# Kernel optimization log

Measured on AMD Instinct MI355X. Metric: run time of the kernel, lower is better.

## Reference

```python
import jax, jax.numpy as jnp
import numpy as np

N, E, G = 16384, 65536, 512
T, FIN, FOUT = 4, 128, 32
_DEG_HIST = np.array([1.0, 2.0, 3.0, 4.0])
AVG_LOG = float((np.log(np.arange(4) + 1.0) * _DEG_HIST).sum() / _DEG_HIST.sum())


def _bn(x, g, b, eps=1e-5):
    # BatchNorm1d in training mode: biased batch stats
    m = x.mean(0)
    v = x.var(0)
    return (x - m) * jax.lax.rsqrt(v + eps) * g + b


def _pna_conv(x, edge_index, ea_raw, We_c, be_c, Wpre, bpre, Wpost, bpost, Wlin, blin):
    src, dst = edge_index[0], edge_index[1]
    ea = ea_raw @ We_c + be_c                                   # conv-internal edge encoder [E,FIN]
    xt = jnp.broadcast_to(x[:, None, :], (N, T, FIN))           # towers share input (divide_input=False)
    h = jnp.concatenate([xt[dst], xt[src],
                         jnp.broadcast_to(ea[:, None, :], (E, T, FIN))], axis=-1)  # [E,T,3*FIN]
    m = jnp.einsum('etf,tfg->etg', h, Wpre) + bpre              # per-tower pre-NN [E,T,FIN]
    deg = jnp.clip(jax.ops.segment_sum(jnp.ones((E,), x.dtype), dst, N), 1.0)
    inv = (1.0 / deg)[:, None, None]
    mean = jax.ops.segment_sum(m, dst, N) * inv
    mean2 = jax.ops.segment_sum(m * m, dst, N) * inv
    std = jnp.sqrt(jax.nn.relu(mean2 - mean * mean) + 1e-5)
    mn = jax.ops.segment_min(m, dst, N)
    mx = jax.ops.segment_max(m, dst, N)
    mn = jnp.where(jnp.isfinite(mn), mn, 0.0)
    mx = jnp.where(jnp.isfinite(mx), mx, 0.0)
    agg = jnp.concatenate([mean, mn, mx, std], axis=-1)         # [N,T,4*FIN]
    s = (jnp.log(deg + 1.0) / AVG_LOG)[:, None, None]           # amplification scaler
    out = jnp.concatenate([agg, agg * s, agg / s], axis=-1)     # identity|amp|attenuation [N,T,12*FIN]
    out = jnp.concatenate([xt, out], axis=-1)                   # [N,T,13*FIN]
    out = jnp.einsum('ntf,tfg->ntg', out, Wpost) + bpost        # per-tower post-NN [N,T,FOUT]
    return out.reshape(N, T * FOUT) @ Wlin + blin               # tower mixing [N,FIN]


def setup_inputs() -> dict:
    key = jax.random.key(0)
    ks = jax.random.split(key, 24)
    def rn(k, shape, scale=0.05):
        return jax.random.normal(k, shape, dtype=jnp.float32) * scale
    return dict(
        x=jax.random.normal(ks[0], (N, 11), jnp.float32),
        edge_attr=jax.random.uniform(ks[1], (E, 4), jnp.float32),
        edge_index=jax.random.randint(ks[2], (2, E), 0, N),
        batch=jnp.sort(jax.random.randint(ks[3], (N,), 0, G)),
        Wa=rn(ks[4], (11, FIN), 0.2), ba=rn(ks[5], (FIN,)),
        We=rn(ks[6], (4, FIN), 0.2), be=rn(ks[7], (FIN,)),
        We_conv=rn(ks[8], (3, FIN, FIN)), be_conv=rn(ks[9], (3, FIN)),
        Wpre=rn(ks[10], (3, T, 3 * FIN, FIN)), bpre=rn(ks[11], (3, T, FIN)),
        Wpost=rn(ks[12], (3, T, 13 * FIN, FOUT)), bpost=rn(ks[13], (3, T, FOUT)),
        Wlin=rn(ks[14], (3, FIN, FIN)), blin=rn(ks[15], (3, FIN)),
        bng=1.0 + rn(ks[16], (3, FIN)), bnb=rn(ks[17], (3, FIN)),
        W1=rn(ks[18], (FIN, 64), 0.1), b1=rn(ks[19], (64,)),
        hg=1.0 + rn(ks[20], (64,)), hb=rn(ks[21], (64,)),
        W2=rn(ks[22], (64, 1), 0.1), b2=rn(ks[23], (1,)),
    )


def reference(x, edge_attr, edge_index, batch, Wa, ba, We, be,
              We_conv, be_conv, Wpre, bpre, Wpost, bpost, Wlin, blin,
              bng, bnb, W1, b1, hg, hb, W2, b2):
    h = jax.nn.relu(x @ Wa + ba)
    ea = jax.nn.relu(edge_attr @ We + be)
    for l in range(3):
        h = jax.nn.relu(_bn(_pna_conv(h, edge_index, ea, We_conv[l], be_conv[l],
                                      Wpre[l], bpre[l], Wpost[l], bpost[l],
                                      Wlin[l], blin[l]), bng[l], bnb[l]))
    cnt = jnp.clip(jax.ops.segment_sum(jnp.ones((N,), h.dtype), batch, G), 1.0)
    pooled = jax.ops.segment_sum(h, batch, G) / cnt[:, None]    # global_mean_pool
    z = jax.nn.relu(pooled @ W1 + b1)
    z = _bn(z, hg, hb)
    return (z @ W2 + b2).reshape(-1)
```

## Files before the change

kernel.cpp:

```cpp
#include <hip/hip_runtime.h>
#include <hip/hip_bf16.h>

#define DEVFN static __device__ __forceinline__

constexpr int NN = 16384;
constexpr int EE = 65536;
constexpr int GG = 512;
constexpr float AVG_LOG_F = 1.0227308671603782f;

typedef _Float16 hfrag __attribute__((ext_vector_type(8)));
typedef __attribute__((ext_vector_type(4))) float f4;
typedef __attribute__((ext_vector_type(8))) unsigned short us8v;

DEVFN unsigned short f2h(float f) {
  _Float16 h = (_Float16)f;
  unsigned short r; __builtin_memcpy(&r, &h, 2); return r;
}
DEVFN float h2f(unsigned short s) {
  _Float16 h; __builtin_memcpy(&h, &s, 2); return (float)h;
}

DEVFN float4 ld4hf(const unsigned short* p) {
  ushort4 u = *(const ushort4*)p;
  float4 r;
  r.x = h2f(u.x); r.y = h2f(u.y); r.z = h2f(u.z); r.w = h2f(u.w);
  return r;
}
DEVFN void ld8hf(const unsigned short* p, float* o) {
  us8v v = *(const us8v*)p;
#pragma unroll
  for (int i = 0; i < 8; ++i) o[i] = h2f(v[i]);
}

DEVFN int swk(int row, int k) {
  return (k & ~31) + ((((k >> 3) & 3) ^ ((row >> 1) & 3)) << 3) + (k & 7);
}

DEVFN void gll16(const unsigned short* g, unsigned short* l) {
  __builtin_amdgcn_global_load_lds(
      (__attribute__((address_space(1))) void*)g,
      (__attribute__((address_space(3))) void*)l, 16, 0, 0);
}

struct AuxP {
  const float* p0;
  const float* p1;
  const float* p2;
  const float* p3;
  const float* p4;
};

__global__ __launch_bounds__(256) void abc_gemm(
    const unsigned short* __restrict__ hbf, const unsigned short* __restrict__ preABT_l,
    unsigned short* __restrict__ AB,
    const unsigned short* __restrict__ eaf, const unsigned short* __restrict__ foldT_l,
    const float* __restrict__ bfold_l, unsigned short* __restrict__ Mb)
{
  __shared__ __align__(16) unsigned short S[16384];
  unsigned short* AhS = S;
  unsigned short* BhS = S + 8192;

  const int bid = blockIdx.x;
  const unsigned short* Abase;
  const unsigned short* Wbase;
  const float* bias = nullptr;
  unsigned short* Cu;
  int ldc, bn;
  long long bm;
  if (bid < 1024) {
    const int z = bid >> 8, y = (bid >> 7) & 1, xm = bid & 127;
    Abase = hbf;
    Wbase = preABT_l + (size_t)z * 256 * 128;
    Cu = AB + (size_t)z * NN * 256;
    ldc = 256; bn = y * 128; bm = (long long)xm * 128;
  } else {
    const int idx = bid - 1024;
    const int z = idx >> 9, xm = idx & 511;
    Abase = eaf;
    Wbase = foldT_l + (size_t)z * 128 * 128;
    bias = bfold_l + z * 128;
    Cu = Mb + (size_t)z * EE * 128;
    ldc = 128; bn = 0; bm = (long long)xm * 128;
  }

  const int tid = threadIdx.x;
  const int w = tid >> 6;
  const int lane = tid & 63;
  const int quad = lane >> 4;
  const int c16 = lane & 15;
  const int srow = lane >> 2;
  const int sslot = (lane & 3) << 3;

  f4 acc[2][8];
#pragma unroll
  for (int mt = 0; mt < 2; ++mt)
#pragma unroll
    for (int nt = 0; nt < 8; ++nt) acc[mt][nt] = (f4){0.f, 0.f, 0.f, 0.f};

  const unsigned short* whp = Wbase + (long long)(bn + srow) * 128 + sslot;
  const unsigned short* ahp = Abase + (bm + srow) * 128 + sslot;
  const int swr8 = ((quad ^ ((c16 >> 1) & 3)) << 3);

  auto stage = [&](int bi, int k0) {
#pragma unroll
    for (int ch = w; ch < 8; ch += 4) {
      gll16(ahp + (long long)ch * 16 * 128 + k0, AhS + bi * 4096 + ch * 512);
      gll16(whp + (long long)ch * 16 * 128 + k0, BhS + bi * 4096 + ch * 512);
    }
  };
  auto fragmfma = [&](int bi) {
    hfrag ah[2];
#pragma unroll
    for (int mt = 0; mt < 2; ++mt)
      ah[mt] = *(const hfrag*)&AhS[bi * 4096 + (w * 32 + mt * 16 + c16) * 32 + swr8];
#pragma unroll
    for (int nt = 0; nt < 8; ++nt) {
      hfrag bh = *(const hfrag*)&BhS[bi * 4096 + (nt * 16 + c16) * 32 + swr8];
#pragma unroll
      for (int mt = 0; mt < 2; ++mt)
        acc[mt][nt] = __builtin_amdgcn_mfma_f32_16x16x32_f16(ah[mt], bh, acc[mt][nt], 0, 0, 0);
    }
  };

  stage(0, 0);
  __syncthreads();
#pragma unroll
  for (int kt = 0; kt < 4; ++kt) {
    const int bi = kt & 1;
    if (kt < 3) stage(bi ^ 1, (kt + 1) << 5);
    fragmfma(bi);
    __syncthreads();
  }

#pragma unroll
  for (int nt = 0; nt < 8; ++nt) {
    const int colL = nt * 16 + c16;
    const float bv = bias ? bias[colL] : 0.f;
#pragma unroll
    for (int mt = 0; mt < 2; ++mt) {
#pragma unroll
      for (int r = 0; r < 4; ++r) {
        const int row = w * 32 + mt * 16 + quad * 4 + r;
        S[row * 128 + colL] = f2h(acc[mt][nt][r] + bv);
      }
    }
  }
  __syncthreads();
#pragma unroll
  for (int p = 0; p < 8; ++p) {
    const int row = p * 16 + (tid >> 4);
    const int co = (tid & 15) * 8;
    *(uint4*)&Cu[(bm + row) * ldc + bn + co] = *(const uint4*)&S[row * 128 + co];
  }
}

template <int ASRC, int NT, bool BIAS, bool RELU, bool OHALF>
__global__ __launch_bounds__(256) void mgemm(
    const void* __restrict__ Av, const unsigned short* __restrict__ WT,
    const float* __restrict__ bias,
    float* __restrict__ C, AuxP aux,
    int Nc, int K, int lda, int ldc,
    long long bsA, long long bsW, long long bsC, int bsBias)
{
  constexpr bool COPYA = (ASRC == 1);
  constexpr int BST = NT * 16 * 32;

  const int z = blockIdx.z;
  WT += (long long)z * bsW;
  if (BIAS) bias += (long long)z * bsBias;
  float* Cf = C + (OHALF ? 0 : (long long)z * bsC);
  unsigned short* Cu = (unsigned short*)C + (OHALF ? (long long)z * bsC : 0);

  __shared__ __align__(16) unsigned short AhS[2 * 128 * 32];
  __shared__ __align__(16) unsigned short BhS[2 * BST];

  const int tid = threadIdx.x;
  const long long bm = (long long)blockIdx.x * 128;
  const int bn = blockIdx.y * (NT * 16);
  const int w = tid >> 6;
  const int lane = tid & 63;
  const int quad = lane >> 4;
  const int c16 = lane & 15;
  const int srow = lane >> 2;
  const int sslot = (lane & 3) << 3;

  const int arow = tid >> 1;
  const int sel = tid & 1;
  const long long rowsrc = bm + arow;

  f4 acc[2][NT];
#pragma unroll
  for (int mt = 0; mt < 2; ++mt)
#pragma unroll
    for (int nt = 0; nt < NT; ++nt) acc[mt][nt] = (f4){0.f, 0.f, 0.f, 0.f};

  const unsigned short* whp = WT + (long long)(bn + srow) * K + sslot;

  const unsigned short* ahp = nullptr;
  if (COPYA || ASRC == 3)
    ahp = (const unsigned short*)Av + (long long)z * bsA + (bm + srow) * (long long)lda + sslot;

  float invdc = 1.f;
  float sv = 0.f, iv = 0.f;
  const float* apA = nullptr;
  const unsigned short* Prow_base = nullptr;
  if (ASRC == 3) {
    Prow_base = (const unsigned short*)aux.p0 + rowsrc * 384;
    sv = aux.p2[rowsrc];
    iv = aux.p3[rowsrc];
  } else if (ASRC == 4) {
    apA = (const float*)Av + (long long)z * bsA + rowsrc * lda;
    invdc = 1.f / fmaxf(aux.p0[rowsrc], 1.f);
  }
  const int swa = (arow >> 1) & 3;
  const int s0us = arow * 32 + (((2 * sel) ^ swa) << 3);
  const int s1us = arow * 32 + (((2 * sel + 1) ^ swa) << 3);

  const int swr8 = ((quad ^ ((c16 >> 1) & 3)) << 3);

  auto stageB = [&](int bi, int k0) {
#pragma unroll
    for (int ch = w; ch < NT; ch += 4)
      gll16(whp + (long long)ch * 16 * K + k0, BhS + bi * BST + ch * 512);
  };
  auto stageA = [&](int bi, int k0) {
#pragma unroll
    for (int ch = w; ch < 8; ch += 4)
      gll16(ahp + (long long)ch * 16 * lda + k0, AhS + bi * 4096 + ch * 512);
  };
  auto stageLoad = [&](int k0, float* va) {
    const int ck0 = k0 + sel * 16;
    if (ASRC == 3) {
      const unsigned short* Prow = Prow_base + ((ck0 >> 5) * 96) + (ck0 & 31);
      float pid[16], pam[16], pat[16];
      ld8hf(Prow, pid); ld8hf(Prow + 8, pid + 8);
      ld8hf(Prow + 32, pam); ld8hf(Prow + 40, pam + 8);
      ld8hf(Prow + 64, pat); ld8hf(Prow + 72, pat + 8);
#pragma unroll
      for (int i = 0; i < 16; ++i)
        va[i] = pid[i] + sv * pam[i] + iv * pat[i] + aux.p4[ck0 + i];
    } else {
      *(float4*)&va[0] = *(const float4*)(apA + ck0);
      *(float4*)&va[4] = *(const float4*)(apA + ck0 + 4);
      *(float4*)&va[8] = *(const float4*)(apA + ck0 + 8);
      *(float4*)&va[12] = *(const float4*)(apA + ck0 + 12);
    }
  };
  auto stageWrite = [&](int bi, const float* va) {
    hfrag hv0, hv1;
#pragma unroll
    for (int i = 0; i < 16; ++i) {
      float x = va[i];
      if (ASRC == 4) x *= invdc;
      if (i < 8) hv0[i] = (_Float16)x;
      else       hv1[i - 8] = (_Float16)x;
    }
    *(hfrag*)&AhS[bi * 4096 + s0us] = hv0;
    *(hfrag*)&AhS[bi * 4096 + s1us] = hv1;
  };
  auto fragmfma = [&](int bi) {
    hfrag ah[2];
#pragma unroll
    for (int mt = 0; mt < 2; ++mt) {
      const int r = w * 32 + mt * 16 + c16;
      ah[mt] = *(const hfrag*)&AhS[bi * 4096 + r * 32 + swr8];
    }
#pragma unroll
    for (int nt = 0; nt < NT; ++nt) {
      const int r = nt * 16 + c16;
      hfrag bh = *(const hfrag*)&BhS[bi * BST + r * 32 + swr8];
#pragma unroll
      for (int mt = 0; mt < 2; ++mt)
        acc[mt][nt] = __builtin_amdgcn_mfma_f32_16x16x32_f16(ah[mt], bh, acc[mt][nt], 0, 0, 0);
    }
  };

  float va[16];
  const int nk = K >> 5;

  if (COPYA) {
    stageA(0, 0);
    stageB(0, 0);
  } else {
    stageLoad(0, va);
    stageB(0, 0);
    stageWrite(0, va);
  }
  __syncthreads();

  for (int kt = 0; kt < nk; ++kt) {
    const int bi = kt & 1;
    const bool pf = (kt + 1 < nk);
    bool nextds = false;
    if (pf) {
      const int k0 = (kt + 1) << 5;
      stageB(bi ^ 1, k0);
      if (COPYA) {
        stageA(bi ^ 1, k0);
      } else if (ASRC == 3 && k0 >= 128) {
        stageA(bi ^ 1, k0 - 128);
      } else {
        stageLoad(k0, va);
        nextds = true;
      }
    }
    fragmfma(bi);
    if (nextds) stageWrite(bi ^ 1, va);
    __syncthreads();
  }

  float ls[NT], lq[NT];
#pragma unroll
  for (int nt = 0; nt < NT; ++nt) { ls[nt] = 0.f; lq[nt] = 0.f; }
#pragma unroll
  for (int nt = 0; nt < NT; ++nt) {
    int col = bn + nt * 16 + c16;
    if (col >= Nc) continue;
    float bv = BIAS ? bias[col] : 0.f;
#pragma unroll
    for (int mt = 0; mt < 2; ++mt) {
#pragma unroll
      for (int r = 0; r < 4; ++r) {
        long long row = bm + w * 32 + mt * 16 + quad * 4 + r;
        float v = acc[mt][nt][r] + bv;
        if (RELU) v = fmaxf(v, 0.f);
        if (ASRC == 3) { ls[nt] += v; lq[nt] += v * v; }
        if (OHALF) Cu[row * ldc + col] = f2h(v);
        else Cf[row * ldc + col] = v;
      }
    }
  }
  if constexpr (ASRC == 3) {
    float* csum = (float*)AhS;
    float* csq = csum + 128;
    if (tid < 128) { csum[tid] = 0.f; csq[tid] = 0.f; }
    __syncthreads();
#pragma unroll
    for (int nt = 0; nt < NT; ++nt) {
      int col = bn + nt * 16 + c16;
      atomicAdd(&csum[col], ls[nt]);
      atomicAdd(&csq[col], lq[nt]);
    }
    __syncthreads();
    float* colsum = (float*)aux.p1;
    if (tid < 128) {
      atomicAdd(&colsum[tid], csum[tid]);
      atomicAdd(&colsum[128 + tid], csq[tid]);
    }
  }
}

__global__ __launch_bounds__(256) void edge_enc(
    const float* __restrict__ eat, const float* __restrict__ We,
    const float* __restrict__ be, const int* __restrict__ slot_of,
    unsigned short* __restrict__ ef)
{
  int e = blockIdx.x * 2 + (threadIdx.x >> 7);
  int c = threadIdx.x & 127;
  float acc = be[c];
#pragma unroll
  for (int k = 0; k < 4; ++k) acc += eat[e * 4 + k] * We[k * 128 + c];
  long long slot = slot_of[e];
  ef[slot * 128 + swk((int)slot, c)] = f2h(fmaxf(acc, 0.f));
}

__global__ void count_deg(const int* __restrict__ dst, int* __restrict__ degi)
{
  int e = blockIdx.x * 256 + threadIdx.x;
  if (e < EE) atomicAdd(&degi[dst[e]], 1);
}

__global__ __launch_bounds__(1024) void scan_k(const int* __restrict__ degi,
                                               int* __restrict__ row_off,
                                               int* __restrict__ cursor,
                                               float* __restrict__ s_arr,
                                               float* __restrict__ invs)
{
  __shared__ int tsum[1024];
  int t = threadIdx.x;
  int local[16];
  int base = t * 16;
  int s = 0;
#pragma unroll
  for (int i = 0; i < 16; ++i) { local[i] = s; s += degi[base + i]; }
  tsum[t] = s;
  __syncthreads();
  for (int off = 1; off < 1024; off <<= 1) {
    int v = (t >= off) ? tsum[t - off] : 0;
    __syncthreads();
    tsum[t] += v;
    __syncthreads();
  }
  int prev = (t == 0) ? 0 : tsum[t - 1];
#pragma unroll
  for (int i = 0; i < 16; ++i) {
    int start = prev + local[i];
    row_off[base + i] = start;
    cursor[base + i] = start;
    int cnt = degi[base + i];
    float degc = fmaxf((float)cnt, 1.f);
    float sv = logf(degc + 1.f) / AVG_LOG_F;
    s_arr[base + i] = sv;
    invs[base + i] = 1.f / sv;
  }
  if (t == 1023) row_off[NN] = tsum[1023];
}

__global__ void scatter_k(const int* __restrict__ src, const int* __restrict__ dst,
                          int* __restrict__ cursor,
                          int* __restrict__ slot_of, int* __restrict__ esrc)
{
  int e = blockIdx.x * 256 + threadIdx.x;
  if (e >= EE) return;
  int d = dst[e];
  int slot = atomicAdd(&cursor[d], 1);
  slot_of[e] = slot;
  esrc[slot] = src[e];
}

__global__ __launch_bounds__(512) void fold_w(const float* __restrict__ We_conv,
                                              const float* __restrict__ Wpre,
                                              float* __restrict__ Wfold)
{
  int k = blockIdx.x & 127, l = blockIdx.x >> 7;
  int t = threadIdx.x >> 7, f = threadIdx.x & 127;
  const float* wc = We_conv + (long long)(l * 128 + k) * 128;
  const float* wp = Wpre + ((long long)((l * 4 + t) * 384 + 256)) * 128 + f;
  float acc = 0.f;
  for (int j = 0; j < 128; ++j) acc += wc[j] * wp[(long long)j * 128];
  Wfold[((long long)(l * 128 + k)) * 512 + threadIdx.x] = acc;
}

__global__ __launch_bounds__(512) void fold_b(const float* __restrict__ be_conv,
                                              const float* __restrict__ Wpre,
                                              const float* __restrict__ bpre,
                                              float* __restrict__ bfold)
{
  int l = blockIdx.x;
  int t = threadIdx.x >> 7, f = threadIdx.x & 127;
  const float* bc = be_conv + l * 128;
  const float* wp = Wpre + ((long long)((l * 4 + t) * 384 + 256)) * 128 + f;
  float acc = bpre[(l * 4 + t) * 128 + f];
  for (int j = 0; j < 128; ++j) acc += bc[j] * wp[(long long)j * 128];
  bfold[l * 512 + threadIdx.x] = acc;
}

__global__ __launch_bounds__(128) void pack_all(
    const float* __restrict__ Wpre, const float* __restrict__ WfoldF,
    const float* __restrict__ Wpost, const float* __restrict__ Wlin,
    const float* __restrict__ W1,
    const float* __restrict__ x, const float* __restrict__ Wa,
    const float* __restrict__ ba,
    unsigned short* __restrict__ preABT, unsigned short* __restrict__ foldT,
    unsigned short* __restrict__ post3T, unsigned short* __restrict__ linT2,
    unsigned short* __restrict__ w1T, unsigned short* __restrict__ hbf)
{
  const int b = blockIdx.x;
  const int t = threadIdx.x;
  if (b < 3072) {
    int lt = b >> 8, n = b & 255, k = t;
    int row = (n < 128) ? k : (128 + k);
    int f = n & 127;
    float v = Wpre[((long long)(lt * 384 + row)) * 128 + f];
    preABT[((long long)(lt * 256 + n)) * 128 + swk(n, k)] = f2h(v);
  } else if (b < 4608) {
    int b2 = b - 3072;
    int lt = b2 >> 7, n = b2 & 127, k = t;
    int l = lt >> 2, tw = lt & 3;
    float v = WfoldF[((long long)(l * 128 + k)) * 512 + tw * 128 + n];
    foldT[((long long)(lt * 128 + n)) * 128 + swk(n, k)] = f2h(v);
  } else if (b < 6144) {
    int b3 = b - 4608;
    int lt = b3 >> 7, c = b3 & 127;
#pragma unroll
    for (int j = 0; j < 4; ++j) {
      int r = t + 128 * j;
      float v = 0.f;
      if (c < 96)
        v = Wpost[((long long)(lt * 1664 + 128 + (c >> 5) * 512 + r)) * 32 + (c & 31)];
      post3T[((long long)(lt * 128 + c)) * 512 + swk(c, r)] = f2h(v);
    }
  } else if (b < 6528) {
    int b4 = b - 6144;
    int l = b4 >> 7, n = b4 & 127, k = t;
    float v = Wlin[((long long)(l * 128 + k)) * 128 + n];
    linT2[((long long)(l * 128 + n)) * 256 + swk(n, k)] = f2h(v);
  } else if (b < 6912) {
    int b5 = b - 6528;
    int l = b5 >> 7, kk = b5 & 127, o = t;
    float acc = 0.f;
    for (int c = 0; c < 128; ++c) {
      float wx = Wpost[((long long)((l * 4 + (c >> 5)) * 1664 + kk)) * 32 + (c & 31)];
      acc += wx * Wlin[((long long)(l * 128 + c)) * 128 + o];
    }
    linT2[((long long)(l * 128 + o)) * 256 + swk(o, 128 + kk)] = f2h(acc);
  } else if (b < 6976) {
    int n = b - 6912, k = t;
    w1T[(long long)n * 128 + swk(n, k)] = f2h(W1[k * 64 + n]);
  } else {
    int n = b - 6976, c = t;
    float acc = ba[c];
#pragma unroll
    for (int k = 0; k < 11; ++k) acc += x[n * 11 + k] * Wa[k * 128 + c];
    hbf[((long long)n << 7) + swk(n, c)] = f2h(fmaxf(acc, 0.f));
  }
}

__global__ __launch_bounds__(256) void aggregate_ct(
    const unsigned short* __restrict__ ABb, const unsigned short* __restrict__ Mb,
    const int* __restrict__ row_off, const int* __restrict__ esrc,
    unsigned short* __restrict__ aggs)
{
  const int tid = threadIdx.x;
  const int c8 = (tid & 15) << 3;
  const int z = (tid >> 4) & 3;
  const int n = blockIdx.x * 4 + (tid >> 6);
  const unsigned short* M = Mb + (long long)z * EE * 128;
  const unsigned short* ABs = ABb + (long long)z * NN * 256;
  unsigned short* ag = aggs + (long long)z * NN * 512;
  const int beg = row_off[n], end = row_off[n + 1];
  const int cnt = end - beg;
  const float degc = fmaxf((float)cnt, 1.0f);
  float aval[8];
  ld8hf(&ABs[(long long)n * 256 + c8], aval);

  float sum[8], sq[8], mn[8], mx[8];
#pragma unroll
  for (int j = 0; j < 8; ++j) {
    sum[j] = 0.f; sq[j] = 0.f; mn[j] = INFINITY; mx[j] = -INFINITY;
  }

  auto upd = [&](const float* mv, const float* bv) {
#pragma unroll
    for (int j = 0; j < 8; ++j) {
      float m = aval[j] + bv[j] + mv[j];
      sum[j] += m; sq[j] += m * m;
      mn[j] = fminf(mn[j], m); mx[j] = fmaxf(mx[j], m);
    }
  };

  for (int s0 = beg; s0 < end; s0 += 4) {
    const int e1 = min(s0 + 1, end - 1);
    const int e2 = min(s0 + 2, end - 1);
    const int e3 = min(s0 + 3, end - 1);
    const int sA = esrc[s0], sB = esrc[e1], sC = esrc[e2], sD = esrc[e3];
    float mA[8], mB[8], mC[8], mD[8], bA[8], bB[8], bC[8], bD[8];
    ld8hf(&M[(long long)s0 * 128 + c8], mA);
    ld8hf(&M[(long long)e1 * 128 + c8], mB);
    ld8hf(&M[(long long)e2 * 128 + c8], mC);
    ld8hf(&M[(long long)e3 * 128 + c8], mD);
    ld8hf(&ABs[(long long)sA * 256 + 128 + c8], bA);
    ld8hf(&ABs[(long long)sB * 256 + 128 + c8], bB);
    ld8hf(&ABs[(long long)sC * 256 + 128 + c8], bC);
    ld8hf(&ABs[(long long)sD * 256 + 128 + c8], bD);
    upd(mA, bA);
    if (s0 + 1 < end) upd(mB, bB);
    if (s0 + 2 < end) upd(mC, bC);
    if (s0 + 3 < end) upd(mD, bD);
  }

  const float inv = 1.0f / degc;
  us8v omean, omin, omax, ostd;
#pragma unroll
  for (int j = 0; j < 8; ++j) {
    float mean = sum[j] * inv;
    float var = sq[j] * inv - mean * mean;
    float stdv = sqrtf(fmaxf(var, 0.f) + 1e-5f);
    float mnv = (cnt > 0) ? mn[j] : 0.f;
    float mxv = (cnt > 0) ? mx[j] : 0.f;
    omean[j] = f2h(mean);
    omin[j] = f2h(mnv);
    omax[j] = f2h(mxv);
    ostd[j] = f2h(stdv);
  }
  const int sc = swk(n, c8);
  const long long base = (long long)n * 512 + sc;
  *(us8v*)&ag[base] = omean;
  *(us8v*)&ag[base + 128] = omin;
  *(us8v*)&ag[base + 256] = omax;
  *(us8v*)&ag[base + 384] = ostd;
}

__global__ __launch_bounds__(256) void bn_apply(const unsigned short* __restrict__ hn,
                                                const float* __restrict__ cs,
                                                const float* __restrict__ g,
                                                const float* __restrict__ b,
                                                unsigned short* __restrict__ hb)
{
  int idx = blockIdx.x * 256 + threadIdx.x;
  int c = idx & 127, n = idx >> 7;
  float mean = cs[c] * (1.f / 16384.f);
  float var = cs[128 + c] * (1.f / 16384.f) - mean * mean;
  float sc = g[c] * rsqrtf(var + 1e-5f);
  float v = fmaxf(h2f(hn[idx]) * sc + (b[c] - mean * sc), 0.f);
  hb[((long long)n << 7) + swk(n, c)] = f2h(v);
}

__global__ void pool_add(const unsigned short* __restrict__ y, const float* __restrict__ cs,
                         const float* __restrict__ g, const float* __restrict__ b,
                         const int* __restrict__ batch,
                         float* __restrict__ pooled, float* __restrict__ cntf)
{
  int n = blockIdx.x, c = threadIdx.x;
  float mean = cs[c] * (1.f / 16384.f);
  float var = cs[128 + c] * (1.f / 16384.f) - mean * mean;
  float v = fmaxf((h2f(y[(long long)n * 128 + c]) - mean) * rsqrtf(var + 1e-5f) * g[c] + b[c], 0.f);
  int bb = batch[n];
  atomicAdd(&pooled[(long long)bb * 128 + c], v);
  if (c == 0) atomicAdd(&cntf[bb], 1.f);
}

__global__ __launch_bounds__(256) void zstats(const float* __restrict__ z,
                                              float* __restrict__ zm, float* __restrict__ zv)
{
  int j = blockIdx.x;
  float s = 0.f, q = 0.f;
  for (int g = threadIdx.x; g < GG; g += 256) {
    float v = z[g * 64 + j];
    s += v;
    q += v * v;
  }
  __shared__ float ps[256], pq[256];
  ps[threadIdx.x] = s;
  pq[threadIdx.x] = q;
  __syncthreads();
  for (int st = 128; st > 0; st >>= 1) {
    if (threadIdx.x < st) {
      ps[threadIdx.x] += ps[threadIdx.x + st];
      pq[threadIdx.x] += pq[threadIdx.x + st];
    }
    __syncthreads();
  }
  if (threadIdx.x == 0) {
    float m = ps[0] / (float)GG;
    zm[j] = m;
    zv[j] = pq[0] / (float)GG - m * m;
  }
}

__global__ void final_out(const float* __restrict__ z, const float* __restrict__ zm,
                          const float* __restrict__ zv, const float* __restrict__ hg,
                          const float* __restrict__ hb, const float* __restrict__ W2,
                          const float* __restrict__ b2, float* __restrict__ out)
{
  int g = blockIdx.x;
  int j = threadIdx.x;
  float v = (z[g * 64 + j] - zm[j]) * rsqrtf(zv[j] + 1e-5f) * hg[j] + hb[j];
  float t = v * W2[j];
#pragma unroll
  for (int off = 32; off > 0; off >>= 1) t += __shfl_down(t, off);
  if (j == 0) out[g] = t + b2[0];
}

extern "C" void kernel_launch(void* const* d_in, const int* in_sizes, int n_in,
                              void* d_out, int out_size, void* d_ws, size_t ws_size,
                              hipStream_t stream)
{
  (void)in_sizes; (void)n_in; (void)out_size;
  const float* x = (const float*)d_in[0];
  const float* eat = (const float*)d_in[1];
  const int* ei = (const int*)d_in[2];
  const int* batch = (const int*)d_in[3];
  const float* Wa = (const float*)d_in[4];
  const float* ba = (const float*)d_in[5];
  const float* We = (const float*)d_in[6];
  const float* be = (const float*)d_in[7];
  const float* We_conv = (const float*)d_in[8];
  const float* be_conv = (const float*)d_in[9];
  const float* Wpre = (const float*)d_in[10];
  const float* bpre = (const float*)d_in[11];
  const float* Wpost = (const float*)d_in[12];
  const float* bpost = (const float*)d_in[13];
  const float* Wlin = (const float*)d_in[14];
  const float* blin = (const float*)d_in[15];
  const float* bng = (const float*)d_in[16];
  const float* bnb = (const float*)d_in[17];
  const float* W1 = (const float*)d_in[18];
  const float* b1 = (const float*)d_in[19];
  const float* hg = (const float*)d_in[20];
  const float* hb = (const float*)d_in[21];
  const float* W2 = (const float*)d_in[22];
  const float* b2 = (const float*)d_in[23];
  float* out = (float*)d_out;

  const int* srcI = ei;
  const int* dstI = ei + EE;

  char* ws = (char*)d_ws;
  size_t off = 0;
  auto alloc = [&](size_t bytes) -> char* {
    char* p = ws + off;
    off += (bytes + 255) & ~(size_t)255;
    return p;
  };

  unsigned short* hbf = (unsigned short*)alloc((size_t)NN * 128 * 2);
  unsigned short* hn = (unsigned short*)alloc((size_t)NN * 128 * 2);
  unsigned short* eaf = (unsigned short*)alloc((size_t)EE * 128 * 2);
  unsigned short* AB = (unsigned short*)alloc((size_t)4 * NN * 256 * 2);
  char* Mregion = alloc((size_t)4 * EE * 128 * 2);
  unsigned short* Mb = (unsigned short*)Mregion;
  unsigned short* P = (unsigned short*)Mregion;
  unsigned short* aggt = (unsigned short*)alloc((size_t)4 * NN * 512 * 2);
  float* s_arr = (float*)alloc((size_t)NN * 4);
  float* invs = (float*)alloc((size_t)NN * 4);
  int* degi = (int*)alloc((size_t)NN * 4);
  int* cursor = (int*)alloc((size_t)NN * 4);
  int* row_off = (int*)alloc((size_t)(NN + 1) * 4);
  int* slot_of = (int*)alloc((size_t)EE * 4);
  int* esrc = (int*)alloc((size_t)EE * 4);
  float* WfoldF = (float*)alloc((size_t)3 * 128 * 512 * 4);
  float* bfold = (float*)alloc((size_t)3 * 512 * 4);
  unsigned short* preABT = (unsigned short*)alloc((size_t)12 * 256 * 128 * 2);
  unsigned short* foldT = (unsigned short*)alloc((size_t)12 * 128 * 128 * 2);
  unsigned short* post3T = (unsigned short*)alloc((size_t)12 * 128 * 512 * 2);
  unsigned short* linT2 = (unsigned short*)alloc((size_t)3 * 128 * 256 * 2);
  unsigned short* w1T = (unsigned short*)alloc((size_t)64 * 128 * 2);
  float* colstats = (float*)alloc(3 * 256 * 4);
  float* pooled = (float*)alloc((size_t)GG * 128 * 4);
  float* cntf = (float*)alloc((size_t)GG * 4);
  float* zbuf = (float*)alloc((size_t)GG * 64 * 4);
  float* zm = (float*)alloc(64 * 4);
  float* zv = (float*)alloc(64 * 4);

  if (off > ws_size) return;

  hipMemsetAsync(degi, 0, (size_t)NN * 4, stream);
  hipMemsetAsync(colstats, 0, 3 * 256 * 4, stream);
  count_deg<<<EE / 256, 256, 0, stream>>>(dstI, degi);
  scan_k<<<1, 1024, 0, stream>>>(degi, row_off, cursor, s_arr, invs);
  scatter_k<<<EE / 256, 256, 0, stream>>>(srcI, dstI, cursor, slot_of, esrc);

  edge_enc<<<EE / 2, 256, 0, stream>>>(eat, We, be, slot_of, eaf);
  fold_w<<<384, 512, 0, stream>>>(We_conv, Wpre, WfoldF);
  fold_b<<<3, 512, 0, stream>>>(be_conv, Wpre, bpre, bfold);
  pack_all<<<6976 + NN, 128, 0, stream>>>(Wpre, WfoldF, Wpost, Wlin, W1, x, Wa, ba,
                                          preABT, foldT, post3T, linT2, w1T, hbf);

  for (int l = 0; l < 3; ++l) {
    float* cs_l = colstats + l * 256;
    abc_gemm<<<3072, 256, 0, stream>>>(
        hbf, preABT + (size_t)l * 4 * 256 * 128, AB,
        eaf, foldT + (size_t)l * 4 * 128 * 128, bfold + l * 512, Mb);
    aggregate_ct<<<dim3(NN / 4, 1, 1), 256, 0, stream>>>(AB, Mb, row_off, esrc, aggt);
    mgemm<1, 6, false, false, true><<<dim3(NN / 128, 1, 4), 256, 0, stream>>>(
        aggt, post3T + (size_t)l * 4 * 128 * 512, nullptr, (float*)P, AuxP{},
        96, 512, 512, 384, (long long)NN * 512, (long long)128 * 512, 96, 0);
    mgemm<3, 8, true, false, true><<<dim3(NN / 128, 1, 1), 256, 0, stream>>>(
        hbf, linT2 + (size_t)l * 128 * 256, blin + l * 128, (float*)hn,
        AuxP{(const float*)P, cs_l, s_arr, invs, bpost + l * 128},
        128, 256, 128, 128, 0, 0, 0, 0);
    if (l < 2)
      bn_apply<<<NN * 128 / 256, 256, 0, stream>>>(hn, cs_l, bng + l * 128,
                                                   bnb + l * 128, hbf);
  }

  hipMemsetAsync(pooled, 0, (size_t)GG * 128 * 4, stream);
  hipMemsetAsync(cntf, 0, (size_t)GG * 4, stream);
  pool_add<<<NN, 128, 0, stream>>>(hn, colstats + 2 * 256,
                                   bng + 2 * 128, bnb + 2 * 128, batch, pooled, cntf);
  mgemm<4, 4, true, true, false><<<dim3(GG / 128, 1, 1), 256, 0, stream>>>(
      pooled, w1T, b1, zbuf, AuxP{cntf, nullptr, nullptr, nullptr, nullptr},
      64, 128, 128, 64, 0, 0, 0, 0);
  zstats<<<64, 256, 0, stream>>>(zbuf, zm, zv);
  final_out<<<GG, 64, 0, stream>>>(zbuf, zm, zv, hg, hb, W2, b2, out);
}
```

Baseline: 554.1 us.

## Fuse edge-feature GEMM into neighbor aggregation to avoid materializing per-edge messages

Splits the combined GEMM kernel so it only computes the node-side A/B projections, and moves the edge-attribute projection into the aggregation kernel. Each aggregation block computes, per 64-edge chunk of its CSR range, the edge projection with MFMA into LDS and then reduces mean/min/max/std from LDS instead of reading a precomputed per-edge buffer from global memory. This removes writing and rereading a large fp16 edge-message tensor per layer, at the cost of smaller, less efficient GEMM tiles, repeated weight staging per chunk, and extra synchronisation inside the aggregation loop.

```diff
diff --git a/kernel.cpp b/kernel.cpp
--- a/kernel.cpp
+++ b/kernel.cpp
@@ -20,12 +20,6 @@
   _Float16 h; __builtin_memcpy(&h, &s, 2); return (float)h;
 }
 
-DEVFN float4 ld4hf(const unsigned short* p) {
-  ushort4 u = *(const ushort4*)p;
-  float4 r;
-  r.x = h2f(u.x); r.y = h2f(u.y); r.z = h2f(u.z); r.w = h2f(u.w);
-  return r;
-}
 DEVFN void ld8hf(const unsigned short* p, float* o) {
   us8v v = *(const us8v*)p;
 #pragma unroll
@@ -50,38 +44,20 @@
   const float* p4;
 };
 
-__global__ __launch_bounds__(256) void abc_gemm(
+__global__ __launch_bounds__(256) void ab_gemm(
     const unsigned short* __restrict__ hbf, const unsigned short* __restrict__ preABT_l,
-    unsigned short* __restrict__ AB,
-    const unsigned short* __restrict__ eaf, const unsigned short* __restrict__ foldT_l,
-    const float* __restrict__ bfold_l, unsigned short* __restrict__ Mb)
+    unsigned short* __restrict__ AB)
 {
   __shared__ __align__(16) unsigned short S[16384];
   unsigned short* AhS = S;
   unsigned short* BhS = S + 8192;
 
   const int bid = blockIdx.x;
-  const unsigned short* Abase;
-  const unsigned short* Wbase;
-  const float* bias = nullptr;
-  unsigned short* Cu;
-  int ldc, bn;
-  long long bm;
-  if (bid < 1024) {
-    const int z = bid >> 8, y = (bid >> 7) & 1, xm = bid & 127;
-    Abase = hbf;
-    Wbase = preABT_l + (size_t)z * 256 * 128;
-    Cu = AB + (size_t)z * NN * 256;
-    ldc = 256; bn = y * 128; bm = (long long)xm * 128;
-  } else {
-    const int idx = bid - 1024;
-    const int z = idx >> 9, xm = idx & 511;
-    Abase = eaf;
-    Wbase = foldT_l + (size_t)z * 128 * 128;
-    bias = bfold_l + z * 128;
-    Cu = Mb + (size_t)z * EE * 128;
-    ldc = 128; bn = 0; bm = (long long)xm * 128;
-  }
+  const int z = bid >> 8, y = (bid >> 7) & 1, xm = bid & 127;
+  const unsigned short* Wbase = preABT_l + (size_t)z * 256 * 128;
+  unsigned short* Cu = AB + (size_t)z * NN * 256;
+  const int bn = y * 128;
+  const long long bm = (long long)xm * 128;
 
   const int tid = threadIdx.x;
   const int w = tid >> 6;
@@ -98,7 +74,7 @@
     for (int nt = 0; nt < 8; ++nt) acc[mt][nt] = (f4){0.f, 0.f, 0.f, 0.f};
 
   const unsigned short* whp = Wbase + (long long)(bn + srow) * 128 + sslot;
-  const unsigned short* ahp = Abase + (bm + srow) * 128 + sslot;
+  const unsigned short* ahp = hbf + (bm + srow) * 128 + sslot;
   const int swr8 = ((quad ^ ((c16 >> 1) & 3)) << 3);
 
   auto stage = [&](int bi, int k0) {
@@ -135,13 +111,12 @@
 #pragma unroll
   for (int nt = 0; nt < 8; ++nt) {
     const int colL = nt * 16 + c16;
-    const float bv = bias ? bias[colL] : 0.f;
 #pragma unroll
     for (int mt = 0; mt < 2; ++mt) {
 #pragma unroll
       for (int r = 0; r < 4; ++r) {
         const int row = w * 32 + mt * 16 + quad * 4 + r;
-        S[row * 128 + colL] = f2h(acc[mt][nt][r] + bv);
+        S[row * 128 + colL] = f2h(acc[mt][nt][r]);
       }
     }
   }
@@ -150,8 +125,144 @@
   for (int p = 0; p < 8; ++p) {
     const int row = p * 16 + (tid >> 4);
     const int co = (tid & 15) * 8;
-    *(uint4*)&Cu[(bm + row) * ldc + bn + co] = *(const uint4*)&S[row * 128 + co];
-  }
+    *(uint4*)&Cu[(bm + row) * 256 + bn + co] = *(const uint4*)&S[row * 128 + co];
+  }
+}
+
+__global__ __launch_bounds__(256) void aggc(
+    const unsigned short* __restrict__ eaf, const unsigned short* __restrict__ foldT_l,
+    const float* __restrict__ bfold_l, const unsigned short* __restrict__ ABb,
+    const int* __restrict__ row_off, const int* __restrict__ esrc,
+    unsigned short* __restrict__ aggs)
+{
+  __shared__ __align__(16) unsigned short AhS[2 * 2048];
+  __shared__ __align__(16) unsigned short BhS[2 * 4096];
+  __shared__ __align__(16) unsigned short Cl[64 * 128];
+
+  const int z = blockIdx.y;
+  const int n0 = blockIdx.x * 16;
+  const unsigned short* W = foldT_l + (size_t)z * 128 * 128;
+  const float* bias = bfold_l + z * 128;
+  const unsigned short* ABs = ABb + (size_t)z * NN * 256;
+  unsigned short* ag = aggs + (size_t)z * NN * 512;
+
+  const int tid = threadIdx.x;
+  const int w = tid >> 6;
+  const int lane = tid & 63;
+  const int quad = lane >> 4;
+  const int c16 = lane & 15;
+  const int srow = lane >> 2;
+  const int sslot = (lane & 3) << 3;
+  const int swr8 = ((quad ^ ((c16 >> 1) & 3)) << 3);
+
+  const int beg0 = row_off[n0];
+  const int end0 = row_off[n0 + 16];
+
+  const int wk = tid >> 4;
+  const int c8 = (tid & 15) << 3;
+  const int n = n0 + wk;
+  const int beg_n = row_off[n];
+  const int end_n = row_off[n + 1];
+  const int cnt = end_n - beg_n;
+  float aval[8];
+  ld8hf(&ABs[(long long)n * 256 + c8], aval);
+
+  float sum[8], sq[8], mn[8], mx[8];
+#pragma unroll
+  for (int j = 0; j < 8; ++j) {
+    sum[j] = 0.f; sq[j] = 0.f; mn[j] = INFINITY; mx[j] = -INFINITY;
+  }
+  auto upd = [&](const float* cv, const float* bv) {
+#pragma unroll
+    for (int j = 0; j < 8; ++j) {
+      float m = aval[j] + bv[j] + cv[j];
+      sum[j] += m; sq[j] += m * m;
+      mn[j] = fminf(mn[j], m); mx[j] = fmaxf(mx[j], m);
+    }
+  };
+
+  const unsigned short* whp = W + (long long)srow * 128 + sslot;
+
+  for (int c0 = (beg0 & ~7); c0 < end0; c0 += 64) {
+    const unsigned short* ahp = eaf + (long long)(c0 + srow) * 128 + sslot;
+    f4 acc[8];
+#pragma unroll
+    for (int nt = 0; nt < 8; ++nt) acc[nt] = (f4){0.f, 0.f, 0.f, 0.f};
+
+    auto stage = [&](int bi, int k0) {
+      gll16(ahp + (long long)(w * 16) * 128 + k0, AhS + bi * 2048 + w * 512);
+#pragma unroll
+      for (int ch = w; ch < 8; ch += 4)
+        gll16(whp + (long long)ch * 16 * 128 + k0, BhS + bi * 4096 + ch * 512);
+    };
+    stage(0, 0);
+    __syncthreads();
+#pragma unroll
+    for (int kt = 0; kt < 4; ++kt) {
+      const int bi = kt & 1;
+      if (kt < 3) stage(bi ^ 1, (kt + 1) << 5);
+      hfrag ah = *(const hfrag*)&AhS[bi * 2048 + (w * 16 + c16) * 32 + swr8];
+#pragma unroll
+      for (int nt = 0; nt < 8; ++nt) {
+        hfrag bh = *(const hfrag*)&BhS[bi * 4096 + (nt * 16 + c16) * 32 + swr8];
+        acc[nt] = __builtin_amdgcn_mfma_f32_16x16x32_f16(ah, bh, acc[nt], 0, 0, 0);
+      }
+      __syncthreads();
+    }
+#pragma unroll
+    for (int nt = 0; nt < 8; ++nt) {
+      const int col = nt * 16 + c16;
+      const float bv = bias[col];
+#pragma unroll
+      for (int r = 0; r < 4; ++r)
+        Cl[(w * 16 + quad * 4 + r) * 128 + col] = f2h(acc[nt][r] + bv);
+    }
+    __syncthreads();
+
+    const int ce = c0 + 64;
+    const int sb = max(beg_n, c0);
+    const int se = min(end_n, ce);
+    for (int s0 = sb; s0 < se; s0 += 4) {
+      const int e1 = min(s0 + 1, se - 1);
+      const int e2 = min(s0 + 2, se - 1);
+      const int e3 = min(s0 + 3, se - 1);
+      const int sA = esrc[s0], sB = esrc[e1], sC = esrc[e2], sD = esrc[e3];
+      float cA[8], cB[8], cC[8], cD[8], bA[8], bB[8], bC[8], bD[8];
+      ld8hf(&Cl[(s0 - c0) * 128 + c8], cA);
+      ld8hf(&Cl[(e1 - c0) * 128 + c8], cB);
+      ld8hf(&Cl[(e2 - c0) * 128 + c8], cC);
+      ld8hf(&Cl[(e3 - c0) * 128 + c8], cD);
+      ld8hf(&ABs[(long long)sA * 256 + 128 + c8], bA);
+      ld8hf(&ABs[(long long)sB * 256 + 128 + c8], bB);
+      ld8hf(&ABs[(long long)sC * 256 + 128 + c8], bC);
+      ld8hf(&ABs[(long long)sD * 256 + 128 + c8], bD);
+      upd(cA, bA);
+      if (s0 + 1 < se) upd(cB, bB);
+      if (s0 + 2 < se) upd(cC, bC);
+      if (s0 + 3 < se) upd(cD, bD);
+    }
+    __syncthreads();
+  }
+
+  const float degc = fmaxf((float)cnt, 1.0f);
+  const float inv = 1.0f / degc;
+  us8v omean, omin, omax, ostd;
+#pragma unroll
+  for (int j = 0; j < 8; ++j) {
+    float mean = sum[j] * inv;
+    float var = sq[j] * inv - mean * mean;
+    float stdv = sqrtf(fmaxf(var, 0.f) + 1e-5f);
+    omean[j] = f2h(mean);
+    omin[j] = f2h((cnt > 0) ? mn[j] : 0.f);
+    omax[j] = f2h((cnt > 0) ? mx[j] : 0.f);
+    ostd[j] = f2h(stdv);
+  }
+  const int sc = swk(n, c8);
+  const long long base = (long long)n * 512 + sc;
+  *(us8v*)&ag[base] = omean;
+  *(us8v*)&ag[base + 128] = omin;
+  *(us8v*)&ag[base + 256] = omax;
+  *(us8v*)&ag[base + 384] = ostd;
 }
 
 template <int ASRC, int NT, bool BIAS, bool RELU, bool OHALF>
@@ -504,81 +615,6 @@
     for (int k = 0; k < 11; ++k) acc += x[n * 11 + k] * Wa[k * 128 + c];
     hbf[((long long)n << 7) + swk(n, c)] = f2h(fmaxf(acc, 0.f));
   }
-}
-
-__global__ __launch_bounds__(256) void aggregate_ct(
-    const unsigned short* __restrict__ ABb, const unsigned short* __restrict__ Mb,
-    const int* __restrict__ row_off, const int* __restrict__ esrc,
-    unsigned short* __restrict__ aggs)
-{
-  const int tid = threadIdx.x;
-  const int c8 = (tid & 15) << 3;
-  const int z = (tid >> 4) & 3;
-  const int n = blockIdx.x * 4 + (tid >> 6);
-  const unsigned short* M = Mb + (long long)z * EE * 128;
-  const unsigned short* ABs = ABb + (long long)z * NN * 256;
-  unsigned short* ag = aggs + (long long)z * NN * 512;
-  const int beg = row_off[n], end = row_off[n + 1];
-  const int cnt = end - beg;
-  const float degc = fmaxf((float)cnt, 1.0f);
-  float aval[8];
-  ld8hf(&ABs[(long long)n * 256 + c8], aval);
-
-  float sum[8], sq[8], mn[8], mx[8];
-#pragma unroll
-  for (int j = 0; j < 8; ++j) {
-    sum[j] = 0.f; sq[j] = 0.f; mn[j] = INFINITY; mx[j] = -INFINITY;
-  }
-
-  auto upd = [&](const float* mv, const float* bv) {
-#pragma unroll
-    for (int j = 0; j < 8; ++j) {
-      float m = aval[j] + bv[j] + mv[j];
-      sum[j] += m; sq[j] += m * m;
-      mn[j] = fminf(mn[j], m); mx[j] = fmaxf(mx[j], m);
-    }
-  };
-
-  for (int s0 = beg; s0 < end; s0 += 4) {
-    const int e1 = min(s0 + 1, end - 1);
-    const int e2 = min(s0 + 2, end - 1);
-    const int e3 = min(s0 + 3, end - 1);
-    const int sA = esrc[s0], sB = esrc[e1], sC = esrc[e2], sD = esrc[e3];
-    float mA[8], mB[8], mC[8], mD[8], bA[8], bB[8], bC[8], bD[8];
-    ld8hf(&M[(long long)s0 * 128 + c8], mA);
-    ld8hf(&M[(long long)e1 * 128 + c8], mB);
-    ld8hf(&M[(long long)e2 * 128 + c8], mC);
-    ld8hf(&M[(long long)e3 * 128 + c8], mD);
-    ld8hf(&ABs[(long long)sA * 256 + 128 + c8], bA);
-    ld8hf(&ABs[(long long)sB * 256 + 128 + c8], bB);
-    ld8hf(&ABs[(long long)sC * 256 + 128 + c8], bC);
-    ld8hf(&ABs[(long long)sD * 256 + 128 + c8], bD);
-    upd(mA, bA);
-    if (s0 + 1 < end) upd(mB, bB);
-    if (s0 + 2 < end) upd(mC, bC);
-    if (s0 + 3 < end) upd(mD, bD);
-  }
-
-  const float inv = 1.0f / degc;
-  us8v omean, omin, omax, ostd;
-#pragma unroll
-  for (int j = 0; j < 8; ++j) {
-    float mean = sum[j] * inv;
-    float var = sq[j] * inv - mean * mean;
-    float stdv = sqrtf(fmaxf(var, 0.f) + 1e-5f);
-    float mnv = (cnt > 0) ? mn[j] : 0.f;
-    float mxv = (cnt > 0) ? mx[j] : 0.f;
-    omean[j] = f2h(mean);
-    omin[j] = f2h(mnv);
-    omax[j] = f2h(mxv);
-    ostd[j] = f2h(stdv);
-  }
-  const int sc = swk(n, c8);
-  const long long base = (long long)n * 512 + sc;
-  *(us8v*)&ag[base] = omean;
-  *(us8v*)&ag[base + 128] = omin;
-  *(us8v*)&ag[base + 256] = omax;
-  *(us8v*)&ag[base + 384] = ostd;
 }
 
 __global__ __launch_bounds__(256) void bn_apply(const unsigned short* __restrict__ hn,
@@ -696,11 +732,9 @@
 
   unsigned short* hbf = (unsigned short*)alloc((size_t)NN * 128 * 2);
   unsigned short* hn = (unsigned short*)alloc((size_t)NN * 128 * 2);
-  unsigned short* eaf = (unsigned short*)alloc((size_t)EE * 128 * 2);
+  unsigned short* eaf = (unsigned short*)alloc((size_t)(EE + 128) * 128 * 2);
   unsigned short* AB = (unsigned short*)alloc((size_t)4 * NN * 256 * 2);
-  char* Mregion = alloc((size_t)4 * EE * 128 * 2);
-  unsigned short* Mb = (unsigned short*)Mregion;
-  unsigned short* P = (unsigned short*)Mregion;
+  unsigned short* P = (unsigned short*)alloc((size_t)NN * 384 * 2);
   unsigned short* aggt = (unsigned short*)alloc((size_t)4 * NN * 512 * 2);
   float* s_arr = (float*)alloc((size_t)NN * 4);
   float* invs = (float*)alloc((size_t)NN * 4);
@@ -739,10 +773,10 @@
 
   for (int l = 0; l < 3; ++l) {
     float* cs_l = colstats + l * 256;
-    abc_gemm<<<3072, 256, 0, stream>>>(
-        hbf, preABT + (size_t)l * 4 * 256 * 128, AB,
-        eaf, foldT + (size_t)l * 4 * 128 * 128, bfold + l * 512, Mb);
-    aggregate_ct<<<dim3(NN / 4, 1, 1), 256, 0, stream>>>(AB, Mb, row_off, esrc, aggt);
+    ab_gemm<<<1024, 256, 0, stream>>>(hbf, preABT + (size_t)l * 4 * 256 * 128, AB);
+    aggc<<<dim3(NN / 16, 4), 256, 0, stream>>>(
+        eaf, foldT + (size_t)l * 4 * 128 * 128, bfold + l * 512,
+        AB, row_off, esrc, aggt);
     mgemm<1, 6, false, false, true><<<dim3(NN / 128, 1, 4), 256, 0, stream>>>(
         aggt, post3T + (size_t)l * 4 * 128 * 512, nullptr, (float*)P, AuxP{},
         96, 512, 512, 384, (long long)NN * 512, (long long)128 * 512, 96, 0);
```

After: 670.5 us. 1.21x slower.
